# Performance work log

Measured on AMD Instinct MI355X. Metric: run time of the kernel, lower is better.

The kernel has to match this reference:

```python
import jax, jax.numpy as jnp
import numpy as np

D_MODEL = 512
PROJ = 2 * D_MODEL  # 1024
N_STATES = 32
KSIZE = 4
LN_EPS = 1e-3  # keras LayerNormalization default epsilon


def setup_inputs() -> dict:
    key = jax.random.key(0)
    ks = jax.random.split(key, 16)
    B, L = 2, 2048
    s_in = 1.0 / np.sqrt(D_MODEL)
    s_pr = 1.0 / np.sqrt(PROJ)
    x = jax.random.normal(ks[0], (B, L, D_MODEL), dtype=jnp.float32)
    # LayerNorm params
    ln_gamma = jnp.ones((D_MODEL,), jnp.float32)
    ln_beta = jnp.zeros((D_MODEL,), jnp.float32)
    # dense1 / dense2: d_model -> proj
    W1 = jax.random.normal(ks[1], (D_MODEL, PROJ), jnp.float32) * s_in
    b1 = jnp.zeros((PROJ,), jnp.float32)
    W2 = jax.random.normal(ks[2], (D_MODEL, PROJ), jnp.float32) * s_in
    b2 = jnp.zeros((PROJ,), jnp.float32)
    # depthwise causal conv1d: kernel (K, 1, PROJ) in WIO layout, groups=PROJ
    conv_k = jax.random.normal(ks[3], (KSIZE, 1, PROJ), jnp.float32) * 0.5
    conv_b = jnp.zeros((PROJ,), jnp.float32)
    # SSM params
    A_log = jnp.log(jnp.broadcast_to(jnp.arange(1, N_STATES + 1, dtype=jnp.float32), (PROJ, N_STATES)))
    D_skip = jnp.ones((PROJ,), jnp.float32)
    WB = jax.random.normal(ks[4], (PROJ, N_STATES), jnp.float32) * s_pr
    bB = jnp.zeros((N_STATES,), jnp.float32)
    WC = jax.random.normal(ks[5], (PROJ, N_STATES), jnp.float32) * s_pr
    bC = jnp.zeros((N_STATES,), jnp.float32)
    Wd = jax.random.normal(ks[6], (PROJ, PROJ), jnp.float32) * s_pr
    bd = jnp.zeros((PROJ,), jnp.float32)
    # dense3: proj -> d_model
    W3 = jax.random.normal(ks[7], (PROJ, D_MODEL), jnp.float32) * s_pr
    b3 = jnp.zeros((D_MODEL,), jnp.float32)
    return dict(x=x, ln_gamma=ln_gamma, ln_beta=ln_beta, W1=W1, b1=b1, W2=W2, b2=b2,
                conv_k=conv_k, conv_b=conv_b, A_log=A_log, D_skip=D_skip,
                WB=WB, bB=bB, WC=WC, bC=bC, Wd=Wd, bd=bd, W3=W3, b3=b3)


def _layernorm(x, gamma, beta):
    mu = jnp.mean(x, axis=-1, keepdims=True)
    var = jnp.mean(jnp.square(x - mu), axis=-1, keepdims=True)
    return (x - mu) * jax.lax.rsqrt(var + LN_EPS) * gamma + beta


def _causal_dwconv(x, k, b):
    # x: [B,L,C], k: [K,1,C], depthwise causal conv (left-pad K-1)
    y = jax.lax.conv_general_dilated(
        x, k, window_strides=(1,), padding=[(KSIZE - 1, 0)],
        dimension_numbers=('NWC', 'WIO', 'NWC'), feature_group_count=PROJ)
    return y + b


def _selective_scan(u, delta, A, Bm, Cm, D_skip):
    # u, delta: [B,L,D]; A: [D,N]; Bm, Cm: [B,L,N]; D_skip: [D]
    deltaA = jnp.einsum('bld,dn->bldn', delta, A)                 # [B,L,D,N]
    deltaBu = jnp.einsum('bld,bld,bln->bldn', delta, u, Bm)        # [B,L,D,N]
    # shift deltaA left by one along L, zero at the end (pad trick in source)
    shifted = jnp.concatenate([deltaA[:, 1:], jnp.zeros_like(deltaA[:, :1])], axis=1)
    # reversed cumsum along L, then exp
    e = jnp.exp(jnp.flip(jnp.cumsum(jnp.flip(shifted, axis=1), axis=1), axis=1))
    xs = jnp.cumsum(deltaBu * e, axis=1) / (e + 1e-12)
    y = jnp.einsum('bldn,bln->bld', xs, Cm)
    return y + u * D_skip


def reference(x, ln_gamma, ln_beta, W1, b1, W2, b2, conv_k, conv_b,
              A_log, D_skip, WB, bB, WC, bC, Wd, bd, W3, b3):
    h = _layernorm(x, ln_gamma, ln_beta)
    x1 = h @ W1 + b1                      # [B,L,PROJ]
    x1 = _causal_dwconv(x1, conv_k, conv_b)
    x1 = jax.nn.silu(x1)
    A = -jnp.exp(A_log)                    # [PROJ,N]
    Cm = x1 @ WC + bC                      # [B,L,N]
    Bm = x1 @ WB + bB                      # [B,L,N]
    delta = jax.nn.softplus(x1 @ Wd + bd)  # [B,L,PROJ]
    y = _selective_scan(x1, delta, A, Bm, Cm, D_skip)
    x2 = jax.nn.silu(h @ W2 + b2)
    out = (y * x2) @ W3 + b3 + x           # residual; dropout is identity at inference
    return out
```

## Files before the change

kernel.cpp:

```cpp
#include <hip/hip_runtime.h>
#include <stdint.h>

#define L_SEQ 2048
#define BATCH 2
#define DMODEL 512
#define PROJ 1024
#define NST 32
#define NCAT 1152
#define ROWS (BATCH*L_SEQ)
#define THRESH 50.0f

typedef float f32x4 __attribute__((ext_vector_type(4)));
typedef short short8 __attribute__((ext_vector_type(8)));

__device__ inline float bf2f(unsigned short u){ uint32_t x=((uint32_t)u)<<16; float f; __builtin_memcpy(&f,&x,4); return f; }
__device__ inline unsigned short f2bf(float f){ uint32_t x; __builtin_memcpy(&x,&f,4); uint32_t r=x+0x7FFFu+((x>>16)&1u); return (unsigned short)(r>>16); }
__device__ inline float siluf(float x){ return x/(1.f+__expf(-x)); }
__device__ inline float softplusf(float x){ return x>20.f? x : log1pf(__expf(x)); }

#define AS1(p) ((const __attribute__((address_space(1))) void*)(p))
#define AS3(p) ((__attribute__((address_space(3))) void*)(p))

__global__ __launch_bounds__(256)
void prep_kernel(const float* __restrict__ W1, const float* __restrict__ b1,
                 const float* __restrict__ W2, const float* __restrict__ b2,
                 const float* __restrict__ Wd, const float* __restrict__ bd,
                 const float* __restrict__ WB, const float* __restrict__ bB,
                 const float* __restrict__ WC, const float* __restrict__ bC,
                 const float* __restrict__ W3,
                 unsigned short* __restrict__ W12t, unsigned short* __restrict__ Wcatt,
                 unsigned short* __restrict__ W3t, float* __restrict__ bias12,
                 float* __restrict__ biascat)
{
  int i = blockIdx.x*256 + threadIdx.x;
  const int nA = 2048*512;
  const int nB = NCAT*1024;
  const int nC = 512*1024;
  if (i < nA) {
    int n = i >> 9, k = i & 511;
    float v = (n < 1024) ? W1[k*1024 + n] : W2[k*1024 + (n-1024)];
    W12t[i] = f2bf(v);
    return;
  }
  i -= nA;
  if (i < nB) {
    int n = i >> 10, k = i & 1023;
    float v;
    if (n < 1024) v = Wd[k*1024 + n];
    else if (n < 1056) v = WB[k*32 + (n-1024)];
    else if (n < 1088) v = WC[k*32 + (n-1056)];
    else v = 0.f;
    Wcatt[i] = f2bf(v);
    return;
  }
  i -= nB;
  if (i < nC) {
    int n = i >> 10, k = i & 1023;
    W3t[i] = f2bf(W3[k*512 + n]);
    return;
  }
  i -= nC;
  if (i < 2048) { bias12[i] = (i < 1024) ? b1[i] : b2[i-1024]; return; }
  i -= 2048;
  if (i < NCAT) {
    biascat[i] = (i < 1024) ? bd[i] : (i < 1056) ? bB[i-1024] : (i < 1088) ? bC[i-1056] : 0.f;
  }
}

__global__ __launch_bounds__(256)
void ln_kernel(const float* __restrict__ x, const float* __restrict__ gamma,
               const float* __restrict__ beta, unsigned short* __restrict__ H)
{
  int row = blockIdx.x*4 + (threadIdx.x >> 6);
  int lane = threadIdx.x & 63;
  const float4* xr = (const float4*)(x + (size_t)row*DMODEL);
  float4 v0 = xr[lane];
  float4 v1 = xr[lane+64];
  float s = v0.x+v0.y+v0.z+v0.w + v1.x+v1.y+v1.z+v1.w;
  float q = v0.x*v0.x+v0.y*v0.y+v0.z*v0.z+v0.w*v0.w
          + v1.x*v1.x+v1.y*v1.y+v1.z*v1.z+v1.w*v1.w;
#pragma unroll
  for (int m=32;m>0;m>>=1){ s += __shfl_xor(s,m); q += __shfl_xor(q,m); }
  float mu = s*(1.f/DMODEL);
  float var = q*(1.f/DMODEL) - mu*mu;
  float rs = rsqrtf(var + 1e-3f);
  int c0 = lane*4, c1 = 256 + lane*4;
  float4 g0 = *(const float4*)&gamma[c0]; float4 g1 = *(const float4*)&gamma[c1];
  float4 t0 = *(const float4*)&beta[c0];  float4 t1 = *(const float4*)&beta[c1];
  ushort4 o0, o1;
  o0.x = f2bf((v0.x-mu)*rs*g0.x + t0.x);
  o0.y = f2bf((v0.y-mu)*rs*g0.y + t0.y);
  o0.z = f2bf((v0.z-mu)*rs*g0.z + t0.z);
  o0.w = f2bf((v0.w-mu)*rs*g0.w + t0.w);
  o1.x = f2bf((v1.x-mu)*rs*g1.x + t1.x);
  o1.y = f2bf((v1.y-mu)*rs*g1.y + t1.y);
  o1.z = f2bf((v1.z-mu)*rs*g1.z + t1.z);
  o1.w = f2bf((v1.w-mu)*rs*g1.w + t1.w);
  *(ushort4*)&H[(size_t)row*DMODEL + c0] = o0;
  *(ushort4*)&H[(size_t)row*DMODEL + c1] = o1;
}

template<int BM, int BN, int WR, int WC, int MODE>
__global__ __launch_bounds__(256)
void gemm_bt(const unsigned short* __restrict__ A, const unsigned short* __restrict__ Bt,
             void* __restrict__ Cv, const float* __restrict__ bias,
             const float* __restrict__ res, int M, int N, int K)
{
  constexpr int BMW = BM/WR, BNW = BN/WC;
  constexpr int AM = BMW/16, AN = BNW/16;
  constexpr int ASEG = BM*4, BSEG = BN*4;
  __shared__ unsigned short As[2][BM*32];
  __shared__ unsigned short Bs[2][BN*32];
  int tid = threadIdx.x;
  int lane = tid & 63, wid = tid >> 6;
  int wm = wid / WC, wn = wid % WC;
  int m0 = blockIdx.x*BM, n0 = blockIdx.y*BN;

  f32x4 acc[AM][AN];
#pragma unroll
  for (int i=0;i<AM;i++)
#pragma unroll
    for (int j=0;j<AN;j++)
#pragma unroll
      for (int e=0;e<4;e++) acc[i][j][e] = 0.f;

  auto stage = [&](int buf, int k0){
#pragma unroll
    for (int j=0;j<ASEG/256;j++){
      int s = tid + j*256;
      int row = s >> 2, kc = ((s & 3) ^ (row & 3)) * 8;
      __builtin_amdgcn_global_load_lds(AS1(&A[(size_t)(m0+row)*K + k0 + kc]),
          AS3(&As[buf][(size_t)(wid*64 + j*256)*8]), 16, 0, 0);
    }
#pragma unroll
    for (int j=0;j<BSEG/256;j++){
      int s = tid + j*256;
      int row = s >> 2, kc = ((s & 3) ^ (row & 3)) * 8;
      __builtin_amdgcn_global_load_lds(AS1(&Bt[(size_t)(n0+row)*K + k0 + kc]),
          AS3(&Bs[buf][(size_t)(wid*64 + j*256)*8]), 16, 0, 0);
    }
  };

  stage(0, 0);
  int cur = 0;
  int r = lane & 15, kb = lane >> 4;
  int kbx = kb ^ (r & 3);
  for (int k0 = 0; k0 < K; k0 += 32) {
    __syncthreads();
    if (k0 + 32 < K) stage(cur^1, k0 + 32);
    short8 af[AM], bfr[AN];
#pragma unroll
    for (int i=0;i<AM;i++) af[i]  = *(const short8*)&As[cur][((wm*BMW + i*16 + r)*4 + kbx)*8];
#pragma unroll
    for (int j=0;j<AN;j++) bfr[j] = *(const short8*)&Bs[cur][((wn*BNW + j*16 + r)*4 + kbx)*8];
#pragma unroll
    for (int i=0;i<AM;i++)
#pragma unroll
      for (int j=0;j<AN;j++)
        acc[i][j] = __builtin_amdgcn_mfma_f32_16x16x32_bf16(af[i], bfr[j], acc[i][j], 0,0,0);
    cur ^= 1;
  }

  int rr = (lane >> 4)*4, cc = lane & 15;
#pragma unroll
  for (int i=0;i<AM;i++)
#pragma unroll
    for (int j=0;j<AN;j++) {
      int col = n0 + wn*BNW + j*16 + cc;
      float bv = bias[col];
#pragma unroll
      for (int e=0;e<4;e++) {
        int row = m0 + wm*BMW + i*16 + rr + e;
        float v = acc[i][j][e] + bv;
        if (MODE == 0) {
          ((unsigned short*)Cv)[(size_t)row*N + col] = f2bf(v);
        } else if (MODE == 2) {
          if (col < 1024) v = softplusf(v);
          ((float*)Cv)[(size_t)row*N + col] = v;
        } else {
          v += res[(size_t)row*N + col];
          ((float*)Cv)[(size_t)row*N + col] = v;
        }
      }
    }
}

__global__ __launch_bounds__(256)
void conv_silu_kernel(const unsigned short* __restrict__ P12, const float* __restrict__ ck,
                      const float* __restrict__ cb, unsigned short* __restrict__ ubf,
                      unsigned short* __restrict__ x2bf)
{
  int gid = blockIdx.x*256 + threadIdx.x;
  int c4 = gid & 511;
  int row = gid >> 9;
  int l = row & (L_SEQ-1);
  if (c4 < 256) {
    int c = c4*4;
    float4 bv = *(const float4*)&cb[c];
    float r0=bv.x, r1=bv.y, r2=bv.z, r3=bv.w;
#pragma unroll
    for (int t=0;t<4;t++){
      int lsrc = l - 3 + t;
      if (lsrc >= 0) {
        ushort4 xv = *(const ushort4*)&P12[(size_t)(row-3+t)*2048 + c];
        float4 kv = *(const float4*)&ck[t*PROJ + c];
        r0 = fmaf(bf2f(xv.x),kv.x,r0);
        r1 = fmaf(bf2f(xv.y),kv.y,r1);
        r2 = fmaf(bf2f(xv.z),kv.z,r2);
        r3 = fmaf(bf2f(xv.w),kv.w,r3);
      }
    }
    ushort4 o;
    o.x=f2bf(siluf(r0)); o.y=f2bf(siluf(r1)); o.z=f2bf(siluf(r2)); o.w=f2bf(siluf(r3));
    *(ushort4*)&ubf[(size_t)row*PROJ + c] = o;
  } else {
    int c = (c4-256)*4;
    ushort4 xv = *(const ushort4*)&P12[(size_t)row*2048 + 1024 + c];
    ushort4 o;
    o.x=f2bf(siluf(bf2f(xv.x))); o.y=f2bf(siluf(bf2f(xv.y)));
    o.z=f2bf(siluf(bf2f(xv.z))); o.w=f2bf(siluf(bf2f(xv.w)));
    *(ushort4*)&x2bf[(size_t)row*PROJ + c] = o;
  }
}

__global__ __launch_bounds__(256)
void dtrans_kernel(const float* __restrict__ P3, float* __restrict__ deltaT)
{
  __shared__ float tile[32][33];
  int bz = blockIdx.z;
  int l0t = blockIdx.x*32, d0t = blockIdx.y*32;
  int lx = threadIdx.x & 31, ly = threadIdx.x >> 5;
#pragma unroll
  for (int i=0;i<4;i++)
    tile[ly+i*8][lx] = P3[(size_t)(bz*L_SEQ + l0t + ly + i*8)*NCAT + d0t + lx];
  __syncthreads();
#pragma unroll
  for (int i=0;i<4;i++)
    deltaT[(size_t)(bz*PROJ + d0t + ly + i*8)*L_SEQ + l0t + lx] = tile[lx][ly+i*8];
}

__global__ __launch_bounds__(256)
void tsum_kernel(const float* __restrict__ deltaT, float* __restrict__ sufshT,
                 int* __restrict__ l0out)
{
  int G = blockIdx.x;
  const float* row = deltaT + (size_t)G*L_SEQ;
  int t = threadIdx.x;
  float4 v0 = *(const float4*)&row[t*8];
  float4 v1 = *(const float4*)&row[t*8+4];
  float vals[8] = {v0.x,v0.y,v0.z,v0.w,v1.x,v1.y,v1.z,v1.w};
  float part = 0.f;
#pragma unroll
  for (int i=0;i<8;i++) part += vals[i];
  __shared__ float ps[256];
  ps[t] = part; __syncthreads();
  for (int off=1; off<256; off<<=1){
    float v = (t >= off) ? ps[t-off] : 0.f;
    __syncthreads();
    ps[t] += v;
    __syncthreads();
  }
  float T = ps[255];
  float prefx = ps[t] - part;
  float run = prefx; int cnt = 0; float out[8];
#pragma unroll
  for (int i=0;i<8;i++){
    float suf_l = T - run;
    cnt += (suf_l >= THRESH) ? 1 : 0;
    run += vals[i];
    out[i] = T - run;
  }
  *(float4*)&sufshT[(size_t)G*L_SEQ + t*8]     = make_float4(out[0],out[1],out[2],out[3]);
  *(float4*)&sufshT[(size_t)G*L_SEQ + t*8 + 4] = make_float4(out[4],out[5],out[6],out[7]);
  __shared__ int cs[256];
  cs[t] = cnt; __syncthreads();
  for (int off=128; off>0; off>>=1){ if (t < off) cs[t] += cs[t+off]; __syncthreads(); }
  if (t == 0) {
    int total = cs[0];
    l0out[G] = total > 0 ? total-1 : 0;
  }
}

__global__ __launch_bounds__(256)
void scan_kernel(const float* __restrict__ deltaT, const float* __restrict__ sufshT,
                 const float* __restrict__ P3, const unsigned short* __restrict__ ubf,
                 const float* __restrict__ A_log, const int* __restrict__ l0arr,
                 float* __restrict__ ystate)
{
  int tid = threadIdx.x;
  int n = tid & 31;
  int G = blockIdx.x*8 + (tid >> 5);
  int b = G >> 10, d = G & 1023;
  float np1 = __expf(A_log[d*NST + n]);
  int myl0 = l0arr[G];
  int base = min(myl0, __shfl_xor(myl0, 32)) & ~7;
  const float* dT = deltaT + (size_t)G*L_SEQ;
  const float* sT = sufshT + (size_t)G*L_SEQ;
  const float* P3b = P3 + (size_t)b*L_SEQ*NCAT + 1024 + n;
  const unsigned short* ub = ubf + (size_t)b*L_SEQ*PROJ + d;
  float* yb = ystate + (size_t)b*L_SEQ*PROJ + d;
  float s = 0.f;
  for (int l = base; l < L_SEQ; l += 8) {
    float4 d0 = *(const float4*)&dT[l];
    float4 d1 = *(const float4*)&dT[l+4];
    float4 f0 = *(const float4*)&sT[l];
    float4 f1 = *(const float4*)&sT[l+4];
    float dl[8] = {d0.x,d0.y,d0.z,d0.w,d1.x,d1.y,d1.z,d1.w};
    float sf[8] = {f0.x,f0.y,f0.z,f0.w,f1.x,f1.y,f1.z,f1.w};
    float uu[8], Bv[8], Cv[8];
#pragma unroll
    for (int t=0;t<8;t++){
      uu[t] = bf2f(ub[(size_t)(l+t)*PROJ]);
      const float* rp = P3b + (size_t)(l+t)*NCAT;
      Bv[t] = rp[0];
      Cv[t] = rp[32];
    }
#pragma unroll
    for (int t=0;t<8;t++){
      float decay = __expf(-dl[t]*np1);
      s = fmaf(decay, s, dl[t]*uu[t]*Bv[t]);
      float gte = 1.f/(1.f + 1e-12f*__expf(np1*sf[t]));
      float contrib = s*gte*Cv[t];
#pragma unroll
      for (int m=16;m>0;m>>=1) contrib += __shfl_xor(contrib, m);
      if (n == 0) yb[(size_t)(l+t)*PROJ] = contrib;
    }
  }
}

__global__ __launch_bounds__(256)
void zmul_kernel(const float* __restrict__ ystate, const unsigned short* __restrict__ ubf,
                 const unsigned short* __restrict__ x2bf, const float* __restrict__ Dskip,
                 unsigned short* __restrict__ zbf)
{
  size_t i = ((size_t)blockIdx.x*256 + threadIdx.x)*4;
  int d = (int)(i & (PROJ-1));
  float4 ys = *(const float4*)&ystate[i];
  ushort4 uu = *(const ushort4*)&ubf[i];
  ushort4 xx = *(const ushort4*)&x2bf[i];
  float4 Dv = *(const float4*)&Dskip[d];
  ushort4 o;
  o.x = f2bf((ys.x + bf2f(uu.x)*Dv.x)*bf2f(xx.x));
  o.y = f2bf((ys.y + bf2f(uu.y)*Dv.y)*bf2f(xx.y));
  o.z = f2bf((ys.z + bf2f(uu.z)*Dv.z)*bf2f(xx.z));
  o.w = f2bf((ys.w + bf2f(uu.w)*Dv.w)*bf2f(xx.w));
  *(ushort4*)&zbf[i] = o;
}

extern "C" void kernel_launch(void* const* d_in, const int* in_sizes, int n_in,
                              void* d_out, int out_size, void* d_ws, size_t ws_size,
                              hipStream_t stream)
{
  const float* x     = (const float*)d_in[0];
  const float* ln_g  = (const float*)d_in[1];
  const float* ln_b  = (const float*)d_in[2];
  const float* W1    = (const float*)d_in[3];
  const float* b1    = (const float*)d_in[4];
  const float* W2    = (const float*)d_in[5];
  const float* b2    = (const float*)d_in[6];
  const float* convk = (const float*)d_in[7];
  const float* convb = (const float*)d_in[8];
  const float* A_log = (const float*)d_in[9];
  const float* Dskip = (const float*)d_in[10];
  const float* WB    = (const float*)d_in[11];
  const float* bB    = (const float*)d_in[12];
  const float* WC    = (const float*)d_in[13];
  const float* bC    = (const float*)d_in[14];
  const float* Wd    = (const float*)d_in[15];
  const float* bd    = (const float*)d_in[16];
  const float* W3    = (const float*)d_in[17];
  const float* b3    = (const float*)d_in[18];

  char* w = (char*)d_ws;
  auto alloc = [&](size_t bytes){ char* p = w; w += (bytes + 255) & ~(size_t)255; return p; };
  unsigned short* Hbf    = (unsigned short*)alloc((size_t)ROWS*DMODEL*2);
  unsigned short* W12t   = (unsigned short*)alloc((size_t)2048*512*2);
  unsigned short* Wcatt  = (unsigned short*)alloc((size_t)NCAT*1024*2);
  unsigned short* W3t    = (unsigned short*)alloc((size_t)512*1024*2);
  float*          bias12 = (float*)alloc(2048*4);
  float*          biascat= (float*)alloc(NCAT*4);
  unsigned short* P12    = (unsigned short*)alloc((size_t)ROWS*2048*2);
  unsigned short* ubf    = (unsigned short*)alloc((size_t)ROWS*PROJ*2);
  unsigned short* x2bf   = (unsigned short*)alloc((size_t)ROWS*PROJ*2);
  float*          P3     = (float*)alloc((size_t)ROWS*NCAT*4);
  float*          deltaT = (float*)alloc((size_t)2048*L_SEQ*4);
  float*          sufshT = (float*)alloc((size_t)2048*L_SEQ*4);
  int*            l0arr  = (int*)alloc(2048*4);
  float*          ystate = (float*)alloc((size_t)ROWS*PROJ*4);
  unsigned short* zbf    = (unsigned short*)alloc((size_t)ROWS*PROJ*2);

  {
    int total = 2048*512 + NCAT*1024 + 512*1024 + 2048 + NCAT;
    prep_kernel<<<(total+255)/256, 256, 0, stream>>>(W1,b1,W2,b2,Wd,bd,WB,bB,WC,bC,W3,
                                                     W12t,Wcatt,W3t,bias12,biascat);
  }
  ln_kernel<<<ROWS/4, 256, 0, stream>>>(x, ln_g, ln_b, Hbf);

  dim3 g1(ROWS/128, 2048/128);
  gemm_bt<128,128,2,2,0><<<g1, 256, 0, stream>>>(Hbf, W12t, P12, bias12, nullptr, ROWS, 2048, DMODEL);

  conv_silu_kernel<<<ROWS*512/256, 256, 0, stream>>>(P12, convk, convb, ubf, x2bf);

  dim3 g2(ROWS/128, NCAT/128);
  gemm_bt<128,128,2,2,2><<<g2, 256, 0, stream>>>(ubf, Wcatt, P3, biascat, nullptr, ROWS, NCAT, PROJ);

  hipMemsetAsync(ystate, 0, (size_t)ROWS*PROJ*4, stream);

  dim3 gt(L_SEQ/32, PROJ/32, BATCH);
  dtrans_kernel<<<gt, 256, 0, stream>>>(P3, deltaT);

  tsum_kernel<<<2048, 256, 0, stream>>>(deltaT, sufshT, l0arr);

  scan_kernel<<<2048/8, 256, 0, stream>>>(deltaT, sufshT, P3, ubf, A_log, l0arr, ystate);

  zmul_kernel<<<(ROWS*PROJ/4)/256, 256, 0, stream>>>(ystate, ubf, x2bf, Dskip, zbf);

  dim3 g3(ROWS/64, DMODEL/128);
  gemm_bt<64,128,1,4,3><<<g3, 256, 0, stream>>>(zbf, W3t, (float*)d_out, b3, x, ROWS, DMODEL, PROJ);
}
```

Baseline: 177.6 us.

## Triple-buffer GEMM LDS staging with explicit vmcnt waits instead of syncthreads

The bf16 MFMA GEMM goes from double to triple buffering of its A/B tiles in LDS, issuing loads two k-steps ahead. It replaces __syncthreads with a partial s_waitcnt vmcnt on the outstanding global-to-LDS loads plus a raw s_barrier, so the newest stage can stay in flight during compute. Per-thread source pointers are precomputed and advanced by 32 each stage, which removes address arithmetic from the loop. The cost is more LDS per block, which may reduce occupancy, and the correctness depends on the hand-chosen vmcnt values matching the number of loads each thread issues.

```diff
diff --git a/kernel.cpp b/kernel.cpp
--- a/kernel.cpp
+++ b/kernel.cpp
@@ -20,6 +20,14 @@
 
 #define AS1(p) ((const __attribute__((address_space(1))) void*)(p))
 #define AS3(p) ((__attribute__((address_space(3))) void*)(p))
+
+template<int N> __device__ inline void wait_vmcnt(){
+  if constexpr (N==0)      asm volatile("s_waitcnt vmcnt(0)" ::: "memory");
+  else if constexpr (N==3) asm volatile("s_waitcnt vmcnt(3)" ::: "memory");
+  else if constexpr (N==4) asm volatile("s_waitcnt vmcnt(4)" ::: "memory");
+  else if constexpr (N==6) asm volatile("s_waitcnt vmcnt(6)" ::: "memory");
+  else                     asm volatile("s_waitcnt vmcnt(8)" ::: "memory");
+}
 
 __global__ __launch_bounds__(256)
 void prep_kernel(const float* __restrict__ W1, const float* __restrict__ b1,
@@ -108,9 +116,11 @@
 {
   constexpr int BMW = BM/WR, BNW = BN/WC;
   constexpr int AM = BMW/16, AN = BNW/16;
-  constexpr int ASEG = BM*4, BSEG = BN*4;
-  __shared__ unsigned short As[2][BM*32];
-  __shared__ unsigned short Bs[2][BN*32];
+  constexpr int ASEGI = BM*4/256;
+  constexpr int BSEGI = BN*4/256;
+  constexpr int LPT = ASEGI + BSEGI;
+  __shared__ unsigned short As[3][BM*32];
+  __shared__ unsigned short Bs[3][BN*32];
   int tid = threadIdx.x;
   int lane = tid & 63, wid = tid >> 6;
   int wm = wid / WC, wn = wid % WC;
@@ -124,41 +134,56 @@
 #pragma unroll
       for (int e=0;e<4;e++) acc[i][j][e] = 0.f;
 
-  auto stage = [&](int buf, int k0){
-#pragma unroll
-    for (int j=0;j<ASEG/256;j++){
-      int s = tid + j*256;
-      int row = s >> 2, kc = ((s & 3) ^ (row & 3)) * 8;
-      __builtin_amdgcn_global_load_lds(AS1(&A[(size_t)(m0+row)*K + k0 + kc]),
-          AS3(&As[buf][(size_t)(wid*64 + j*256)*8]), 16, 0, 0);
-    }
-#pragma unroll
-    for (int j=0;j<BSEG/256;j++){
-      int s = tid + j*256;
-      int row = s >> 2, kc = ((s & 3) ^ (row & 3)) * 8;
-      __builtin_amdgcn_global_load_lds(AS1(&Bt[(size_t)(n0+row)*K + k0 + kc]),
-          AS3(&Bs[buf][(size_t)(wid*64 + j*256)*8]), 16, 0, 0);
+  const unsigned short* ap[ASEGI];
+  const unsigned short* bp[BSEGI];
+#pragma unroll
+  for (int j=0;j<ASEGI;j++){
+    int s = tid + j*256;
+    int row = s >> 2, kc = ((s & 3) ^ (row & 3)) * 8;
+    ap[j] = A + (size_t)(m0+row)*K + kc;
+  }
+#pragma unroll
+  for (int j=0;j<BSEGI;j++){
+    int s = tid + j*256;
+    int row = s >> 2, kc = ((s & 3) ^ (row & 3)) * 8;
+    bp[j] = Bt + (size_t)(n0+row)*K + kc;
+  }
+
+  auto stage = [&](int buf){
+#pragma unroll
+    for (int j=0;j<ASEGI;j++){
+      __builtin_amdgcn_global_load_lds(AS1(ap[j]), AS3(&As[buf][(size_t)(wid*64 + j*256)*8]), 16, 0, 0);
+      ap[j] += 32;
+    }
+#pragma unroll
+    for (int j=0;j<BSEGI;j++){
+      __builtin_amdgcn_global_load_lds(AS1(bp[j]), AS3(&Bs[buf][(size_t)(wid*64 + j*256)*8]), 16, 0, 0);
+      bp[j] += 32;
     }
   };
 
-  stage(0, 0);
-  int cur = 0;
+  stage(0);
+  stage(1);
+  int T = K/32;
+  int rb = 0, wb = 2;
   int r = lane & 15, kb = lane >> 4;
   int kbx = kb ^ (r & 3);
-  for (int k0 = 0; k0 < K; k0 += 32) {
-    __syncthreads();
-    if (k0 + 32 < K) stage(cur^1, k0 + 32);
+  for (int t = 0; t < T; ++t) {
+    if (t+1 < T) wait_vmcnt<LPT>();
+    else         wait_vmcnt<0>();
+    __builtin_amdgcn_s_barrier();
+    if (t+2 < T) { stage(wb); wb = (wb==2)?0:wb+1; }
     short8 af[AM], bfr[AN];
 #pragma unroll
-    for (int i=0;i<AM;i++) af[i]  = *(const short8*)&As[cur][((wm*BMW + i*16 + r)*4 + kbx)*8];
-#pragma unroll
-    for (int j=0;j<AN;j++) bfr[j] = *(const short8*)&Bs[cur][((wn*BNW + j*16 + r)*4 + kbx)*8];
+    for (int i=0;i<AM;i++) af[i]  = *(const short8*)&As[rb][((wm*BMW + i*16 + r)*4 + kbx)*8];
+#pragma unroll
+    for (int j=0;j<AN;j++) bfr[j] = *(const short8*)&Bs[rb][((wn*BNW + j*16 + r)*4 + kbx)*8];
 #pragma unroll
     for (int i=0;i<AM;i++)
 #pragma unroll
       for (int j=0;j<AN;j++)
         acc[i][j] = __builtin_amdgcn_mfma_f32_16x16x32_bf16(af[i], bfr[j], acc[i][j], 0,0,0);
-    cur ^= 1;
+    rb = (rb==2)?0:rb+1;
   }
 
   int rr = (lane >> 4)*4, cc = lane & 15;
```

Measured after the change: 178.5 us. Within noise of the previous version (+0.5%).
